# Kernel tuning notes

Hardware: AMD Instinct MI355X
Metric: run time of the kernel (lower is better)

## Reference

```python
import jax, jax.numpy as jnp
import numpy as np

B, T, D, N = 32, 2048, 1024, 1024  # batch, time, feature dim, n_dense


def setup_inputs() -> dict:
    key = jax.random.key(0)
    ks = jax.random.split(key, 8)
    s = 1.0 / np.sqrt(D)
    return {
        "query": jax.random.normal(ks[0], (B, D), jnp.float32),
        "values": jax.random.normal(ks[1], (B, T, D), jnp.float32),
        "W1": jax.random.uniform(ks[2], (D, N), jnp.float32, -s, s),
        "b1": jnp.zeros((N,), jnp.float32),
        "W2": jax.random.uniform(ks[3], (D, N), jnp.float32, -s, s),
        "b2": jnp.zeros((N,), jnp.float32),
        "V": jax.random.uniform(ks[4], (N, 1), jnp.float32, -1.0 / np.sqrt(N), 1.0 / np.sqrt(N)),
        "bV": jnp.zeros((1,), jnp.float32),
    }


def reference(query, values, W1, b1, W2, b2, V, bV):
    # q_proj: [B, 1, N], v_proj: [B, T, N]
    q_proj = (query @ W1 + b1)[:, None, :]
    v_proj = jnp.einsum("btd,dn->btn", values, W2) + b2
    # score: [B, T, 1]
    score = jnp.tanh(q_proj + v_proj) @ V + bV
    attention_weights = jax.nn.softmax(score, axis=1)  # softmax over time
    # context: [B, D]
    context_vector = jnp.sum(attention_weights * values, axis=1)
    return (context_vector, attention_weights)
```

## Files before the change

### kernel.cpp

```cpp
#include <hip/hip_runtime.h>
#include <hip/hip_bf16.h>

#define B_ 32
#define T_ 2048
#define D_ 1024
#define N_ 1024
#define M_ (B_*T_)

#define BM 64
#define BN 128
#define BK 64
#define NTSPLIT 2

typedef short bf16x8 __attribute__((ext_vector_type(8)));
typedef float f32x4 __attribute__((ext_vector_type(4)));
typedef unsigned short us4 __attribute__((ext_vector_type(4)));

__device__ __forceinline__ unsigned short bf16_rn(float x) {
    unsigned u = __float_as_uint(x);
    u += 0x7FFFu + ((u >> 16) & 1u);
    return (unsigned short)(u >> 16);
}

__device__ __forceinline__ void gload_lds16(const void* g, void* l) {
    __builtin_amdgcn_global_load_lds(
        (__attribute__((address_space(1))) void*)(g),
        (__attribute__((address_space(3))) void*)(l), 16, 0, 0);
}

__global__ void k0_w2t(const float* __restrict__ W2,
                       unsigned short* __restrict__ Th) {
    __shared__ float tile[32][33];
    int n0 = blockIdx.x * 32, d0 = blockIdx.y * 32;
    int tx = threadIdx.x & 31, ty = threadIdx.x >> 5;
    #pragma unroll
    for (int i = 0; i < 4; i++) {
        int d = d0 + ty + i * 8;
        tile[ty + i * 8][tx] = W2[d * N_ + n0 + tx];
    }
    __syncthreads();
    #pragma unroll
    for (int i = 0; i < 4; i++) {
        int n = n0 + ty + i * 8;
        Th[n * D_ + d0 + tx] = bf16_rn(tile[tx][ty + i * 8]);
    }
}

__global__ void k0_vals(const float* __restrict__ v,
                        unsigned short* __restrict__ o) {
    size_t i = ((size_t)blockIdx.x * 256 + threadIdx.x) * 8;
    const size_t stride = (size_t)gridDim.x * 256 * 8;
    for (; i < (size_t)M_ * D_; i += stride) {
        float4 a = *(const float4*)(v + i);
        float4 b = *(const float4*)(v + i + 4);
        us4 h0, h1;
        h0[0] = bf16_rn(a.x); h0[1] = bf16_rn(a.y);
        h0[2] = bf16_rn(a.z); h0[3] = bf16_rn(a.w);
        h1[0] = bf16_rn(b.x); h1[1] = bf16_rn(b.y);
        h1[2] = bf16_rn(b.z); h1[3] = bf16_rn(b.w);
        *(us4*)(o + i) = h0;
        *(us4*)(o + i + 4) = h1;
    }
}

__global__ void k1_qproj(const float* __restrict__ query,
                         const float* __restrict__ W1,
                         const float* __restrict__ b1,
                         float* __restrict__ qp) {
    int b = blockIdx.x;
    int n = blockIdx.y * 256 + threadIdx.x;
    const float* q = query + b * D_;
    const float* w = W1 + n;
    float s = 0.f;
    #pragma unroll 8
    for (int d = 0; d < D_; d++) s += q[d] * w[d * N_];
    qp[b * N_ + n] = s + b1[n];
}

__global__ __launch_bounds__(256, 2) void k2_score(
    const unsigned short* __restrict__ Av,
    const unsigned short* __restrict__ W2Th,
    const float* __restrict__ qp,
    const float* __restrict__ b2,
    const float* __restrict__ V,
    float* __restrict__ score) {
    __shared__ unsigned short sAh[BM * BK];
    __shared__ unsigned short sBh[BN * BK];
    __shared__ float red[2 * BM];

    const int tid = threadIdx.x;
    const int lane = tid & 63;
    const int wid = tid >> 6;
    const int wm = wid >> 1, wn = wid & 1;
    const int g = lane >> 4, c16 = lane & 15;

    const int m0 = blockIdx.x * BM;
    const int b = m0 >> 11;
    const int nt0 = blockIdx.y * (N_ / BN / NTSPLIT);

    const int b_rl = lane >> 3;
    const int b_j = lane & 7;

    float rowpart[8];
    #pragma unroll
    for (int i = 0; i < 8; i++) rowpart[i] = 0.f;

    for (int nt = nt0; nt < nt0 + N_ / BN / NTSPLIT; nt++) {
        f32x4 acc[2][4];
        #pragma unroll
        for (int mi = 0; mi < 2; mi++)
            #pragma unroll
            for (int ni = 0; ni < 4; ni++) {
                f32x4 z = {0.f, 0.f, 0.f, 0.f};
                acc[mi][ni] = z;
            }

        for (int kt = 0; kt < D_ / BK; kt++) {
            const int k0 = kt * BK;
            __syncthreads();

            #pragma unroll
            for (int i = 0; i < 4; i++) {
                int r = wid * 32 + i * 8 + b_rl;
                int jj = b_j ^ (r & 7);
                size_t soff = (size_t)(nt * BN + r) * D_ + k0 + jj * 8;
                gload_lds16(W2Th + soff, &sBh[(wid * 32 + i * 8) * 64]);
            }
            #pragma unroll
            for (int i = 0; i < 2; i++) {
                int r = wid * 16 + i * 8 + b_rl;
                int jj = b_j ^ (r & 7);
                size_t soff = (size_t)(m0 + r) * D_ + k0 + jj * 8;
                gload_lds16(Av + soff, &sAh[(wid * 16 + i * 8) * 64]);
            }

            __syncthreads();

            #pragma unroll
            for (int s = 0; s < 2; s++) {
                bf16x8 aH[2], bH[4];
                #pragma unroll
                for (int mi = 0; mi < 2; mi++) {
                    int r = wm * 32 + mi * 16 + c16;
                    int idx = r * 64 + (((s * 4 + g) ^ (r & 7)) << 3);
                    aH[mi] = *(const bf16x8*)&sAh[idx];
                }
                #pragma unroll
                for (int ni = 0; ni < 4; ni++) {
                    int r = wn * 64 + ni * 16 + c16;
                    int idx = r * 64 + (((s * 4 + g) ^ (r & 7)) << 3);
                    bH[ni] = *(const bf16x8*)&sBh[idx];
                }
                #pragma unroll
                for (int mi = 0; mi < 2; mi++)
                    #pragma unroll
                    for (int ni = 0; ni < 4; ni++)
                        acc[mi][ni] = __builtin_amdgcn_mfma_f32_16x16x32_bf16(aH[mi], bH[ni], acc[mi][ni], 0, 0, 0);
            }
        }

        #pragma unroll
        for (int ni = 0; ni < 4; ni++) {
            int n = nt * BN + wn * 64 + ni * 16 + c16;
            float qv = qp[b * N_ + n] + b2[n];
            float Vv = V[n];
            #pragma unroll
            for (int mi = 0; mi < 2; mi++)
                #pragma unroll
                for (int r = 0; r < 4; r++) {
                    rowpart[mi * 4 + r] += tanhf(acc[mi][ni][r] + qv) * Vv;
                }
        }
    }

    #pragma unroll
    for (int i = 0; i < 8; i++) {
        float v = rowpart[i];
        v += __shfl_xor(v, 1);
        v += __shfl_xor(v, 2);
        v += __shfl_xor(v, 4);
        v += __shfl_xor(v, 8);
        rowpart[i] = v;
    }
    if (c16 == 0) {
        #pragma unroll
        for (int mi = 0; mi < 2; mi++)
            #pragma unroll
            for (int r = 0; r < 4; r++)
                red[wn * BM + wm * 32 + mi * 16 + g * 4 + r] = rowpart[mi * 4 + r];
    }
    __syncthreads();
    if (tid < BM) {
        atomicAdd(&score[m0 + tid], red[tid] + red[BM + tid]);
    }
}

__global__ void k3_softmax(float* __restrict__ sw) {
    int b = blockIdx.x;
    float* row = sw + b * T_;
    int tid = threadIdx.x;
    float v[8];
    float lmax = -1e30f;
    #pragma unroll
    for (int i = 0; i < 8; i++) {
        v[i] = row[tid + i * 256];
        lmax = fmaxf(lmax, v[i]);
    }
    #pragma unroll
    for (int d = 1; d < 64; d <<= 1) lmax = fmaxf(lmax, __shfl_xor(lmax, d));
    __shared__ float sm[4], ss[4];
    if ((tid & 63) == 0) sm[tid >> 6] = lmax;
    __syncthreads();
    lmax = fmaxf(fmaxf(sm[0], sm[1]), fmaxf(sm[2], sm[3]));
    float lsum = 0.f;
    #pragma unroll
    for (int i = 0; i < 8; i++) {
        v[i] = expf(v[i] - lmax);
        lsum += v[i];
    }
    #pragma unroll
    for (int d = 1; d < 64; d <<= 1) lsum += __shfl_xor(lsum, d);
    if ((tid & 63) == 0) ss[tid >> 6] = lsum;
    __syncthreads();
    lsum = ss[0] + ss[1] + ss[2] + ss[3];
    float inv = 1.f / lsum;
    #pragma unroll
    for (int i = 0; i < 8; i++) row[tid + i * 256] = v[i] * inv;
}

__global__ void k4_context(const float* __restrict__ values,
                           const float* __restrict__ w,
                           float* __restrict__ ctx) {
    int b = blockIdx.x;
    int dc = blockIdx.y;
    int tc = blockIdx.z;
    int d4 = threadIdx.x & 31;
    int th = threadIdx.x >> 5;
    const float* wrow = w + b * T_;
    int d = dc * 128 + d4 * 4;
    const float* vbase = values + (size_t)b * T_ * D_ + d;
    float4 acc = {0.f, 0.f, 0.f, 0.f};
    int t0 = tc * 256 + th * 32;
    for (int t = t0; t < t0 + 32; t++) {
        float wt = wrow[t];
        float4 vv = *(const float4*)(vbase + (size_t)t * D_);
        acc.x += wt * vv.x;
        acc.y += wt * vv.y;
        acc.z += wt * vv.z;
        acc.w += wt * vv.w;
    }
    __shared__ float4 red4[256];
    red4[threadIdx.x] = acc;
    __syncthreads();
    if (th == 0) {
        float4 s = red4[d4];
        #pragma unroll
        for (int i = 1; i < 8; i++) {
            float4 o = red4[i * 32 + d4];
            s.x += o.x; s.y += o.y; s.z += o.z; s.w += o.w;
        }
        atomicAdd(&ctx[b * D_ + d + 0], s.x);
        atomicAdd(&ctx[b * D_ + d + 1], s.y);
        atomicAdd(&ctx[b * D_ + d + 2], s.z);
        atomicAdd(&ctx[b * D_ + d + 3], s.w);
    }
}

extern "C" void kernel_launch(void* const* d_in, const int* in_sizes, int n_in,
                              void* d_out, int out_size, void* d_ws, size_t ws_size,
                              hipStream_t stream) {
    const float* query  = (const float*)d_in[0];
    const float* values = (const float*)d_in[1];
    const float* W1     = (const float*)d_in[2];
    const float* b1     = (const float*)d_in[3];
    const float* W2     = (const float*)d_in[4];
    const float* b2     = (const float*)d_in[5];
    const float* V      = (const float*)d_in[6];

    float* ctx = (float*)d_out;
    float* weights = (float*)d_out + B_ * D_;

    size_t need = (size_t)N_ * D_ * sizeof(unsigned short)
                + (size_t)B_ * N_ * sizeof(float)
                + (size_t)M_ * D_ * sizeof(unsigned short);
    if (ws_size < need) return;
    unsigned short* Th = (unsigned short*)d_ws;
    float* qp = (float*)(Th + (size_t)N_ * D_);
    unsigned short* Av = (unsigned short*)(qp + (size_t)B_ * N_);

    k0_w2t<<<dim3(N_ / 32, D_ / 32), 256, 0, stream>>>(W2, Th);
    k0_vals<<<2048, 256, 0, stream>>>(values, Av);
    k1_qproj<<<dim3(B_, N_ / 256), 256, 0, stream>>>(query, W1, b1, qp);
    hipMemsetAsync(weights, 0, (size_t)B_ * T_ * sizeof(float), stream);
    k2_score<<<dim3(M_ / BM, NTSPLIT), 256, 0, stream>>>(Av, Th, qp, b2, V, weights);
    k3_softmax<<<B_, 256, 0, stream>>>(weights);
    hipMemsetAsync(ctx, 0, (size_t)B_ * D_ * sizeof(float), stream);
    k4_context<<<dim3(B_, 8, 8), 256, 0, stream>>>(values, weights, ctx);
}
```

Measured before the change: 387.9 us.

## Fuse fp32-to-bf16 conversion of values into score GEMM and drop atomics

Removes the separate pass that converted all of values to bf16. The score GEMM now loads fp32 values directly into LDS and converts them to bf16 in registers before the MFMA. It also remaps workgroup IDs so the two N-halves of the same M tile are scheduled close together, which should help L2 reuse of the A tile. The atomicAdd and memset are replaced by per-half partial score buffers that softmax sums. The costs are double the LDS footprint and A-tile global bytes inside the GEMM, plus extra conversion ALU work in the inner loop.

```diff
diff --git a/kernel.cpp b/kernel.cpp
--- a/kernel.cpp
+++ b/kernel.cpp
@@ -28,6 +28,17 @@
         (__attribute__((address_space(3))) void*)(l), 16, 0, 0);
 }
 
+__device__ __forceinline__ short bf16s(float f) {
+    __hip_bfloat16 h = __float2bfloat16(f);
+    return *reinterpret_cast<short*>(&h);
+}
+__device__ __forceinline__ bf16x8 cvt8(float4 x, float4 y) {
+    bf16x8 r;
+    r[0] = bf16s(x.x); r[1] = bf16s(x.y); r[2] = bf16s(x.z); r[3] = bf16s(x.w);
+    r[4] = bf16s(y.x); r[5] = bf16s(y.y); r[6] = bf16s(y.z); r[7] = bf16s(y.w);
+    return r;
+}
+
 __global__ void k0_w2t(const float* __restrict__ W2,
                        unsigned short* __restrict__ Th) {
     __shared__ float tile[32][33];
@@ -43,23 +54,6 @@
     for (int i = 0; i < 4; i++) {
         int n = n0 + ty + i * 8;
         Th[n * D_ + d0 + tx] = bf16_rn(tile[tx][ty + i * 8]);
-    }
-}
-
-__global__ void k0_vals(const float* __restrict__ v,
-                        unsigned short* __restrict__ o) {
-    size_t i = ((size_t)blockIdx.x * 256 + threadIdx.x) * 8;
-    const size_t stride = (size_t)gridDim.x * 256 * 8;
-    for (; i < (size_t)M_ * D_; i += stride) {
-        float4 a = *(const float4*)(v + i);
-        float4 b = *(const float4*)(v + i + 4);
-        us4 h0, h1;
-        h0[0] = bf16_rn(a.x); h0[1] = bf16_rn(a.y);
-        h0[2] = bf16_rn(a.z); h0[3] = bf16_rn(a.w);
-        h1[0] = bf16_rn(b.x); h1[1] = bf16_rn(b.y);
-        h1[2] = bf16_rn(b.z); h1[3] = bf16_rn(b.w);
-        *(us4*)(o + i) = h0;
-        *(us4*)(o + i + 4) = h1;
     }
 }
 
@@ -78,13 +72,13 @@
 }
 
 __global__ __launch_bounds__(256, 2) void k2_score(
-    const unsigned short* __restrict__ Av,
+    const float* __restrict__ values,
     const unsigned short* __restrict__ W2Th,
     const float* __restrict__ qp,
     const float* __restrict__ b2,
     const float* __restrict__ V,
-    float* __restrict__ score) {
-    __shared__ unsigned short sAh[BM * BK];
+    float* __restrict__ scorep) {
+    __shared__ float sAf[BM * BK];
     __shared__ unsigned short sBh[BN * BK];
     __shared__ float red[2 * BM];
 
@@ -94,12 +88,17 @@
     const int wm = wid >> 1, wn = wid & 1;
     const int g = lane >> 4, c16 = lane & 15;
 
-    const int m0 = blockIdx.x * BM;
+    const int bid = blockIdx.x;
+    const int wgid = ((bid & 7) << 8) | (bid >> 3);
+    const int m0 = (wgid >> 1) * BM;
     const int b = m0 >> 11;
-    const int nt0 = blockIdx.y * (N_ / BN / NTSPLIT);
+    const int half = wgid & 1;
+    const int nt0 = half * (N_ / BN / NTSPLIT);
 
     const int b_rl = lane >> 3;
     const int b_j = lane & 7;
+    const int a_r4 = lane >> 4;
+    const int a_s = lane & 15;
 
     float rowpart[8];
     #pragma unroll
@@ -127,28 +126,32 @@
                 gload_lds16(W2Th + soff, &sBh[(wid * 32 + i * 8) * 64]);
             }
             #pragma unroll
-            for (int i = 0; i < 2; i++) {
-                int r = wid * 16 + i * 8 + b_rl;
-                int jj = b_j ^ (r & 7);
-                size_t soff = (size_t)(m0 + r) * D_ + k0 + jj * 8;
-                gload_lds16(Av + soff, &sAh[(wid * 16 + i * 8) * 64]);
+            for (int i = 0; i < 4; i++) {
+                int row = wid * 16 + i * 4 + a_r4;
+                int cc = a_s ^ (row & 15);
+                size_t soff = (size_t)(m0 + row) * D_ + k0 + cc * 4;
+                gload_lds16(values + soff, &sAf[(wid * 16 + i * 4) * 64]);
             }
 
             __syncthreads();
 
             #pragma unroll
             for (int s = 0; s < 2; s++) {
+                const int j0 = s * 4 + g;
                 bf16x8 aH[2], bH[4];
                 #pragma unroll
                 for (int mi = 0; mi < 2; mi++) {
                     int r = wm * 32 + mi * 16 + c16;
-                    int idx = r * 64 + (((s * 4 + g) ^ (r & 7)) << 3);
-                    aH[mi] = *(const bf16x8*)&sAh[idx];
+                    int c0 = (2 * j0) ^ (r & 15);
+                    int c1 = (2 * j0 + 1) ^ (r & 15);
+                    float4 lo = *(const float4*)&sAf[r * 64 + c0 * 4];
+                    float4 hi = *(const float4*)&sAf[r * 64 + c1 * 4];
+                    aH[mi] = cvt8(lo, hi);
                 }
                 #pragma unroll
                 for (int ni = 0; ni < 4; ni++) {
                     int r = wn * 64 + ni * 16 + c16;
-                    int idx = r * 64 + (((s * 4 + g) ^ (r & 7)) << 3);
+                    int idx = r * 64 + ((j0 ^ (r & 7)) << 3);
                     bH[ni] = *(const bf16x8*)&sBh[idx];
                 }
                 #pragma unroll
@@ -191,19 +194,23 @@
     }
     __syncthreads();
     if (tid < BM) {
-        atomicAdd(&score[m0 + tid], red[tid] + red[BM + tid]);
-    }
-}
-
-__global__ void k3_softmax(float* __restrict__ sw) {
+        scorep[(size_t)half * M_ + m0 + tid] = red[tid] + red[BM + tid];
+    }
+}
+
+__global__ void k3_softmax(const float* __restrict__ sp,
+                           float* __restrict__ sw) {
     int b = blockIdx.x;
+    const float* r0 = sp + b * T_;
+    const float* r1 = sp + M_ + b * T_;
     float* row = sw + b * T_;
     int tid = threadIdx.x;
     float v[8];
     float lmax = -1e30f;
     #pragma unroll
     for (int i = 0; i < 8; i++) {
-        v[i] = row[tid + i * 256];
+        int idx = tid + i * 256;
+        v[i] = r0[idx] + r1[idx];
         lmax = fmaxf(lmax, v[i]);
     }
     #pragma unroll
@@ -282,18 +289,16 @@
 
     size_t need = (size_t)N_ * D_ * sizeof(unsigned short)
                 + (size_t)B_ * N_ * sizeof(float)
-                + (size_t)M_ * D_ * sizeof(unsigned short);
+                + (size_t)NTSPLIT * M_ * sizeof(float);
     if (ws_size < need) return;
     unsigned short* Th = (unsigned short*)d_ws;
     float* qp = (float*)(Th + (size_t)N_ * D_);
-    unsigned short* Av = (unsigned short*)(qp + (size_t)B_ * N_);
+    float* scorep = qp + (size_t)B_ * N_;
 
     k0_w2t<<<dim3(N_ / 32, D_ / 32), 256, 0, stream>>>(W2, Th);
-    k0_vals<<<2048, 256, 0, stream>>>(values, Av);
     k1_qproj<<<dim3(B_, N_ / 256), 256, 0, stream>>>(query, W1, b1, qp);
-    hipMemsetAsync(weights, 0, (size_t)B_ * T_ * sizeof(float), stream);
-    k2_score<<<dim3(M_ / BM, NTSPLIT), 256, 0, stream>>>(Av, Th, qp, b2, V, weights);
-    k3_softmax<<<B_, 256, 0, stream>>>(weights);
+    k2_score<<<(M_ / BM) * NTSPLIT, 256, 0, stream>>>(values, Th, qp, b2, V, scorep);
+    k3_softmax<<<B_, 256, 0, stream>>>(scorep, weights);
     hipMemsetAsync(ctx, 0, (size_t)B_ * D_ * sizeof(float), stream);
     k4_context<<<dim3(B_, 8, 8), 256, 0, stream>>>(values, weights, ctx);
 }
```

After: 354.3 us. 1.09x faster.
